# Performance work log

Measured on AMD Instinct MI355X. Metric: run time of the kernel, lower is better.

The kernel has to match this reference:

```python
import jax, jax.numpy as jnp
import numpy as np

IN_FEATURES = 4096
OUT_FEATURES = 11008
GROUP_SIZE = 128
NUM_GROUPS = IN_FEATURES // GROUP_SIZE


def setup_inputs() -> dict:
    key = jax.random.key(0)
    k1, k2, k3, k4 = jax.random.split(key, 4)
    x = jax.random.normal(k1, (4, 2048, IN_FEATURES), dtype=jnp.float32)
    qweight = jax.random.randint(k2, (OUT_FEATURES, NUM_GROUPS, GROUP_SIZE), 0, 16, dtype=jnp.int32).astype(jnp.int8)
    scales = jax.random.uniform(k3, (OUT_FEATURES, NUM_GROUPS), dtype=jnp.float32) * 0.02
    zeros = jax.random.uniform(k4, (OUT_FEATURES, NUM_GROUPS), dtype=jnp.float32) * 15.0
    return {"x": x, "qweight": qweight, "scales": scales, "zeros": zeros}


def reference(x, qweight, scales, zeros) -> jnp.ndarray:
    # Dequantize: (q - zero) * scale per (out_feature, group), then dense matmul.
    # qweight: [O, G, S], scales/zeros: [O, G] -> weight: [O, in]
    w = (qweight.astype(jnp.float32) - zeros[:, :, None]) * scales[:, :, None]
    w = w.reshape(OUT_FEATURES, IN_FEATURES)
    # x: [B, T, in] @ w.T -> [B, T, out]
    return jnp.einsum('bti,oi->bto', x, w)
```

## Files before the change

kernel.cpp:

```cpp
#include <hip/hip_runtime.h>
#include <hip/hip_bf16.h>
#include <stdint.h>


#define M_DIM 8192
#define K_DIM 4096
#define N_DIM 11008

typedef _Float16 f16x8 __attribute__((ext_vector_type(8)));
typedef float f32x4 __attribute__((ext_vector_type(4)));

__device__ __forceinline__ bool q_is_int8(const void* q) {
  const unsigned* w = (const unsigned*)q;
  unsigned m = 0;
#pragma unroll
  for (int i = 0; i < 16; ++i) m |= w[i] & 0xFFFFFF00u;
  return m != 0u;
}

__global__ void cvt_x_kernel(const float* __restrict__ X, _Float16* __restrict__ Xh, long total) {
  long e = ((long)blockIdx.x * blockDim.x + threadIdx.x) * 8;
  const long stride = (long)gridDim.x * blockDim.x * 8;
  for (; e < total; e += stride) {
    const float4 a = *(const float4*)(X + e);
    const float4 b = *(const float4*)(X + e + 4);
    f16x8 o;
    o[0] = (_Float16)a.x; o[1] = (_Float16)a.y; o[2] = (_Float16)a.z; o[3] = (_Float16)a.w;
    o[4] = (_Float16)b.x; o[5] = (_Float16)b.y; o[6] = (_Float16)b.z; o[7] = (_Float16)b.w;
    *(f16x8*)(Xh + e) = o;
  }
}

__global__ void dequant_w_kernel(const void* __restrict__ qraw,
                                 const float* __restrict__ scales,
                                 const float* __restrict__ zeros,
                                 _Float16* __restrict__ W) {
  const bool is8 = q_is_int8(qraw);
  const long total = (long)N_DIM * K_DIM;
  long e = ((long)blockIdx.x * blockDim.x + threadIdx.x) * 8;
  const long stride = (long)gridDim.x * blockDim.x * 8;
  for (; e < total; e += stride) {
    const long g = e >> 7;
    const float s = scales[g];
    const float z = zeros[g];
    float v[8];
    if (is8) {
      const uint2 p = *(const uint2*)((const uint8_t*)qraw + e);
      const unsigned a = p.x, b = p.y;
      v[0] = (float)(a & 0xFF);         v[1] = (float)((a >> 8) & 0xFF);
      v[2] = (float)((a >> 16) & 0xFF); v[3] = (float)(a >> 24);
      v[4] = (float)(b & 0xFF);         v[5] = (float)((b >> 8) & 0xFF);
      v[6] = (float)((b >> 16) & 0xFF); v[7] = (float)(b >> 24);
    } else {
      const int* qi = (const int*)qraw;
      const int4 p0 = *(const int4*)(qi + e);
      const int4 p1 = *(const int4*)(qi + e + 4);
      v[0] = (float)p0.x; v[1] = (float)p0.y; v[2] = (float)p0.z; v[3] = (float)p0.w;
      v[4] = (float)p1.x; v[5] = (float)p1.y; v[6] = (float)p1.z; v[7] = (float)p1.w;
    }
    f16x8 o;
#pragma unroll
    for (int k = 0; k < 8; ++k) o[k] = (_Float16)((v[k] - z) * s);
    *(f16x8*)(W + e) = o;
  }
}

__global__ __launch_bounds__(512, 2) void gemm_f16_pipe(
    const _Float16* __restrict__ A, const _Float16* __restrict__ B,
    float* __restrict__ C) {
  __shared__ __align__(16) _Float16 As[4][8192];
  __shared__ __align__(16) _Float16 Bs[4][8192];

  const int t = threadIdx.x;
  const int sw = ((blockIdx.x & 7) * 172) + (blockIdx.x >> 3);
  const int bm = sw & 31;
  const int bn = sw >> 5;

  const int w = t >> 6, l = t & 63;
  const int wm = w >> 2, wn = w & 3;
  const int fr = l & 15;
  const int cph = (l >> 4) << 3;

  const int sr = t >> 2;
  const int sc = (t & 3) << 3;
  const _Float16* Ag = A + (size_t)(bm * 256 + sr) * K_DIM + sc;
  const _Float16* Bg = B + (size_t)(bn * 256 + sr) * K_DIM + sc;

  f32x4 acc[8][4] = {};

#define AS1 const __attribute__((address_space(1))) void*
#define AS3 __attribute__((address_space(3))) void*
#define STAGE(kt, bf) do { \
    __builtin_amdgcn_global_load_lds((AS1)(Ag + (kt)), (AS3)(&As[bf][t * 8]), 16, 0, 0); \
    __builtin_amdgcn_global_load_lds((AS1)(Ag + 128 * K_DIM + (kt)), (AS3)(&As[bf][4096 + t * 8]), 16, 0, 0); \
    __builtin_amdgcn_global_load_lds((AS1)(Bg + (kt)), (AS3)(&Bs[bf][t * 8]), 16, 0, 0); \
    __builtin_amdgcn_global_load_lds((AS1)(Bg + 128 * K_DIM + (kt)), (AS3)(&Bs[bf][4096 + t * 8]), 16, 0, 0); \
  } while (0)

#define COMPUTE(bf) do { \
    const _Float16* Ap = &As[bf][(wm * 128 + fr) * 32 + cph]; \
    const _Float16* Bp = &Bs[bf][(wn * 64 + fr) * 32 + cph]; \
    f16x8 af[8]; f16x8 bg[4]; \
    _Pragma("unroll") for (int m = 0; m < 8; ++m) af[m] = *(const f16x8*)(Ap + m * 512); \
    _Pragma("unroll") for (int n = 0; n < 4; ++n) bg[n] = *(const f16x8*)(Bp + n * 512); \
    __builtin_amdgcn_s_setprio(1); \
    _Pragma("unroll") for (int m = 0; m < 8; ++m) \
      _Pragma("unroll") for (int n = 0; n < 4; ++n) \
        acc[m][n] = __builtin_amdgcn_mfma_f32_16x16x32_f16(af[m], bg[n], acc[m][n], 0, 0, 0); \
    __builtin_amdgcn_s_setprio(0); \
  } while (0)

#define WAITV(nimm) asm volatile("s_waitcnt vmcnt(" #nimm ")" ::: "memory")
#define BARRIER() do { __builtin_amdgcn_s_barrier(); asm volatile("" ::: "memory"); } while (0)

  STAGE(0, 0); STAGE(32, 1); STAGE(64, 2);
  WAITV(8);
  BARRIER();

  int kt = 96;
#pragma unroll 1
  for (int it = 0; it < 31; ++it) {
    STAGE(kt, 3);       COMPUTE(0); WAITV(8); BARRIER();
    STAGE(kt + 32, 0);  COMPUTE(1); WAITV(8); BARRIER();
    STAGE(kt + 64, 1);  COMPUTE(2); WAITV(8); BARRIER();
    STAGE(kt + 96, 2);  COMPUTE(3); WAITV(8); BARRIER();
    kt += 128;
  }
  STAGE(4064, 3); COMPUTE(0); WAITV(8); BARRIER();
  COMPUTE(1); WAITV(4); BARRIER();
  COMPUTE(2); WAITV(0); BARRIER();
  COMPUTE(3);

  const int qrow = (l >> 4) * 2;
  float* Cb = C + (size_t)(bm * 256 + wm * 128 + (l >> 4) * 4) * N_DIM + bn * 256 + wn * 64 + fr;
  (void)qrow;
#pragma unroll
  for (int m = 0; m < 8; ++m)
#pragma unroll
    for (int r = 0; r < 4; ++r) {
      float* Cr = Cb + (size_t)(m * 16 + r) * N_DIM;
#pragma unroll
      for (int n = 0; n < 4; ++n) Cr[n * 16] = acc[m][n][r];
    }
#undef STAGE
#undef COMPUTE
#undef WAITV
#undef BARRIER
#undef AS1
#undef AS3
}

extern "C" void kernel_launch(void* const* d_in, const int* in_sizes, int n_in,
                              void* d_out, int out_size, void* d_ws, size_t ws_size,
                              hipStream_t stream) {
  const float* x      = (const float*)d_in[0];
  const void*  qw     = d_in[1];
  const float* scales = (const float*)d_in[2];
  const float* zeros  = (const float*)d_in[3];
  float* out = (float*)d_out;

  const size_t xh_bytes = (size_t)M_DIM * K_DIM * sizeof(_Float16);
  const size_t wh_bytes = (size_t)N_DIM * K_DIM * sizeof(_Float16);
  if (ws_size < xh_bytes + wh_bytes) return;

  _Float16* Xh = (_Float16*)d_ws;
  _Float16* Wh = (_Float16*)((char*)d_ws + xh_bytes);

  cvt_x_kernel<<<2048, 256, 0, stream>>>(x, Xh, (long)M_DIM * K_DIM);
  dequant_w_kernel<<<2048, 256, 0, stream>>>(qw, scales, zeros, Wh);

  gemm_f16_pipe<<<dim3((M_DIM / 256) * (N_DIM / 256)), 512, 0, stream>>>(Xh, Wh, out);
}
```

Before: 1.386 ms.

## Restructure f16 GEMM into 8-phase double-buffered pipeline with swizzled LDS

Replaces the four-stage K=32 ring buffer with two K=64 buffers and an eight-phase schedule. Each phase interleaves partial LDS fragment reads, staggered global-to-LDS loads and a half-tile of MFMAs between barriers. An XOR swizzle on the LDS column chunks is meant to avoid bank conflicts on the wider 64-element rows. The added barriers and the tail-loop wraparound loads (masked kt) increase synchronization and issue a few redundant loads at the end in exchange for finer overlap.

Result: faster. 1.280 ms (-7.7%).

```diff
diff --git a/kernel.cpp b/kernel.cpp
--- a/kernel.cpp
+++ b/kernel.cpp
@@ -65,11 +65,11 @@
   }
 }
 
-__global__ __launch_bounds__(512, 2) void gemm_f16_pipe(
+__global__ __launch_bounds__(512, 2) void gemm_f16_8ph(
     const _Float16* __restrict__ A, const _Float16* __restrict__ B,
     float* __restrict__ C) {
-  __shared__ __align__(16) _Float16 As[4][8192];
-  __shared__ __align__(16) _Float16 Bs[4][8192];
+  __shared__ __align__(16) _Float16 As[2][16384];
+  __shared__ __align__(16) _Float16 Bs[2][16384];
 
   const int t = threadIdx.x;
   const int sw = ((blockIdx.x & 7) * 172) + (blockIdx.x >> 3);
@@ -79,61 +79,99 @@
   const int w = t >> 6, l = t & 63;
   const int wm = w >> 2, wn = w & 3;
   const int fr = l & 15;
-  const int cph = (l >> 4) << 3;
-
-  const int sr = t >> 2;
-  const int sc = (t & 3) << 3;
-  const _Float16* Ag = A + (size_t)(bm * 256 + sr) * K_DIM + sc;
-  const _Float16* Bg = B + (size_t)(bn * 256 + sr) * K_DIM + sc;
+  const int hi = l >> 4;
+  const int sx = fr & 7;
+
+  const int sl0 = ((hi) ^ sx) * 8;
+  const int sl1 = ((4 + hi) ^ sx) * 8;
+  const int arow = (wm * 128 + fr) * 64;
+  const int brow = (wn * 64 + fr) * 64;
+
+  const int tr = t >> 3;
+  const int ss = ((t & 7) ^ (tr & 7)) * 8;
+  const _Float16* Ag = A + (size_t)(bm * 256 + tr) * K_DIM + ss;
+  const _Float16* Bg = B + (size_t)(bn * 256 + tr) * K_DIM + ss;
 
   f32x4 acc[8][4] = {};
+  f16x8 af[4], bg0[4], bg1[4];
 
 #define AS1 const __attribute__((address_space(1))) void*
 #define AS3 __attribute__((address_space(3))) void*
-#define STAGE(kt, bf) do { \
-    __builtin_amdgcn_global_load_lds((AS1)(Ag + (kt)), (AS3)(&As[bf][t * 8]), 16, 0, 0); \
-    __builtin_amdgcn_global_load_lds((AS1)(Ag + 128 * K_DIM + (kt)), (AS3)(&As[bf][4096 + t * 8]), 16, 0, 0); \
-    __builtin_amdgcn_global_load_lds((AS1)(Bg + (kt)), (AS3)(&Bs[bf][t * 8]), 16, 0, 0); \
-    __builtin_amdgcn_global_load_lds((AS1)(Bg + 128 * K_DIM + (kt)), (AS3)(&Bs[bf][4096 + t * 8]), 16, 0, 0); \
-  } while (0)
-
-#define COMPUTE(bf) do { \
-    const _Float16* Ap = &As[bf][(wm * 128 + fr) * 32 + cph]; \
-    const _Float16* Bp = &Bs[bf][(wn * 64 + fr) * 32 + cph]; \
-    f16x8 af[8]; f16x8 bg[4]; \
-    _Pragma("unroll") for (int m = 0; m < 8; ++m) af[m] = *(const f16x8*)(Ap + m * 512); \
-    _Pragma("unroll") for (int n = 0; n < 4; ++n) bg[n] = *(const f16x8*)(Bp + n * 512); \
+#define STAGE_A(b, kt) do { \
+    __builtin_amdgcn_global_load_lds((AS1)(Ag + (kt)),                 (AS3)(&As[b][t * 8]), 16, 0, 0); \
+    __builtin_amdgcn_global_load_lds((AS1)(Ag +  64 * K_DIM + (kt)),   (AS3)(&As[b][4096 + t * 8]), 16, 0, 0); \
+    __builtin_amdgcn_global_load_lds((AS1)(Ag + 128 * K_DIM + (kt)),   (AS3)(&As[b][8192 + t * 8]), 16, 0, 0); \
+    __builtin_amdgcn_global_load_lds((AS1)(Ag + 192 * K_DIM + (kt)),   (AS3)(&As[b][12288 + t * 8]), 16, 0, 0); \
+  } while (0)
+#define STAGE_B_LO(b, kt) do { \
+    __builtin_amdgcn_global_load_lds((AS1)(Bg + (kt)),                 (AS3)(&Bs[b][t * 8]), 16, 0, 0); \
+    __builtin_amdgcn_global_load_lds((AS1)(Bg +  64 * K_DIM + (kt)),   (AS3)(&Bs[b][4096 + t * 8]), 16, 0, 0); \
+  } while (0)
+#define STAGE_B_HI(b, kt) do { \
+    __builtin_amdgcn_global_load_lds((AS1)(Bg + 128 * K_DIM + (kt)),   (AS3)(&Bs[b][8192 + t * 8]), 16, 0, 0); \
+    __builtin_amdgcn_global_load_lds((AS1)(Bg + 192 * K_DIM + (kt)),   (AS3)(&Bs[b][12288 + t * 8]), 16, 0, 0); \
+  } while (0)
+
+#define LDA(b, q, sl) do { \
+    af[0] = *(const f16x8*)(&As[b][arow + (q) * 4096 + (sl)]); \
+    af[1] = *(const f16x8*)(&As[b][arow + (q) * 4096 + 1024 + (sl)]); \
+    af[2] = *(const f16x8*)(&As[b][arow + (q) * 4096 + 2048 + (sl)]); \
+    af[3] = *(const f16x8*)(&As[b][arow + (q) * 4096 + 3072 + (sl)]); \
+  } while (0)
+#define LDB(b, dst, sl) do { \
+    dst[0] = *(const f16x8*)(&Bs[b][brow + (sl)]); \
+    dst[1] = *(const f16x8*)(&Bs[b][brow + 1024 + (sl)]); \
+    dst[2] = *(const f16x8*)(&Bs[b][brow + 2048 + (sl)]); \
+    dst[3] = *(const f16x8*)(&Bs[b][brow + 3072 + (sl)]); \
+  } while (0)
+
+#define MM(q, bgv) do { \
     __builtin_amdgcn_s_setprio(1); \
-    _Pragma("unroll") for (int m = 0; m < 8; ++m) \
+    _Pragma("unroll") for (int mi = 0; mi < 4; ++mi) \
       _Pragma("unroll") for (int n = 0; n < 4; ++n) \
-        acc[m][n] = __builtin_amdgcn_mfma_f32_16x16x32_f16(af[m], bg[n], acc[m][n], 0, 0, 0); \
+        acc[(q) * 4 + mi][n] = __builtin_amdgcn_mfma_f32_16x16x32_f16(af[mi], bgv[n], acc[(q) * 4 + mi][n], 0, 0, 0); \
     __builtin_amdgcn_s_setprio(0); \
   } while (0)
 
-#define WAITV(nimm) asm volatile("s_waitcnt vmcnt(" #nimm ")" ::: "memory")
-#define BARRIER() do { __builtin_amdgcn_s_barrier(); asm volatile("" ::: "memory"); } while (0)
-
-  STAGE(0, 0); STAGE(32, 1); STAGE(64, 2);
-  WAITV(8);
-  BARRIER();
-
-  int kt = 96;
+#define BAR() do { asm volatile("" ::: "memory"); __builtin_amdgcn_s_barrier(); asm volatile("" ::: "memory"); } while (0)
+#define WAITV(n) asm volatile("s_waitcnt vmcnt(" #n ")" ::: "memory")
+
+  STAGE_A(0, 0);
+  STAGE_B_LO(0, 0); STAGE_B_HI(0, 0);
+  STAGE_B_LO(1, 64); STAGE_B_HI(1, 64);
+  WAITV(4);
+  BAR();
+
 #pragma unroll 1
-  for (int it = 0; it < 31; ++it) {
-    STAGE(kt, 3);       COMPUTE(0); WAITV(8); BARRIER();
-    STAGE(kt + 32, 0);  COMPUTE(1); WAITV(8); BARRIER();
-    STAGE(kt + 64, 1);  COMPUTE(2); WAITV(8); BARRIER();
-    STAGE(kt + 96, 2);  COMPUTE(3); WAITV(8); BARRIER();
-    kt += 128;
+  for (int i = 0; i < 32; ++i) {
+    const int ktA1 = i * 128 + 64;
+    const int ktN2 = (i * 128 + 128) & 4095;
+    const int ktN3 = (i * 128 + 192) & 4095;
+    LDA(0, 0, sl0); LDB(0, bg0, sl0);
+    STAGE_A(1, ktA1);
+    BAR(); MM(0, bg0); BAR();
+    LDA(0, 0, sl1); LDB(0, bg1, sl1);
+    BAR(); MM(0, bg1); BAR();
+    LDA(0, 1, sl0);
+    STAGE_B_LO(0, ktN2);
+    BAR(); MM(1, bg0); BAR();
+    LDA(0, 1, sl1);
+    STAGE_B_HI(0, ktN2);
+    BAR(); MM(1, bg1); WAITV(4); BAR();
+    LDA(1, 0, sl0); LDB(1, bg0, sl0);
+    STAGE_A(0, ktN2);
+    BAR(); MM(0, bg0); BAR();
+    LDA(1, 0, sl1); LDB(1, bg1, sl1);
+    BAR(); MM(0, bg1); BAR();
+    LDA(1, 1, sl0);
+    STAGE_B_LO(1, ktN3);
+    BAR(); MM(1, bg0); BAR();
+    LDA(1, 1, sl1);
+    STAGE_B_HI(1, ktN3);
+    BAR(); MM(1, bg1); WAITV(4); BAR();
   }
-  STAGE(4064, 3); COMPUTE(0); WAITV(8); BARRIER();
-  COMPUTE(1); WAITV(4); BARRIER();
-  COMPUTE(2); WAITV(0); BARRIER();
-  COMPUTE(3);
-
-  const int qrow = (l >> 4) * 2;
-  float* Cb = C + (size_t)(bm * 256 + wm * 128 + (l >> 4) * 4) * N_DIM + bn * 256 + wn * 64 + fr;
-  (void)qrow;
+
+  float* Cb = C + (size_t)(bm * 256 + wm * 128 + hi * 4) * N_DIM + bn * 256 + wn * 64 + fr;
 #pragma unroll
   for (int m = 0; m < 8; ++m)
 #pragma unroll
@@ -142,10 +180,14 @@
 #pragma unroll
       for (int n = 0; n < 4; ++n) Cr[n * 16] = acc[m][n][r];
     }
-#undef STAGE
-#undef COMPUTE
+#undef STAGE_A
+#undef STAGE_B_LO
+#undef STAGE_B_HI
+#undef LDA
+#undef LDB
+#undef MM
+#undef BAR
 #undef WAITV
-#undef BARRIER
 #undef AS1
 #undef AS3
 }
@@ -169,5 +211,5 @@
   cvt_x_kernel<<<2048, 256, 0, stream>>>(x, Xh, (long)M_DIM * K_DIM);
   dequant_w_kernel<<<2048, 256, 0, stream>>>(qw, scales, zeros, Wh);
 
-  gemm_f16_pipe<<<dim3((M_DIM / 256) * (N_DIM / 256)), 512, 0, stream>>>(Xh, Wh, out);
-}
+  gemm_f16_8ph<<<dim3((M_DIM / 256) * (N_DIM / 256)), 512, 0, stream>>>(Xh, Wh, out);
+}
```

## Rewrite GEMM mainloop with 32x32x16 MFMA, XOR-swizzled LDS and split staging

Applied to the files above, without the earlier changes.

The f16 GEMM moves from 16x16x32 MFMAs with a 4-stage 32-wide K pipeline to 32x32x16 MFMAs over 64-wide K tiles with double buffering. LDS rows are XOR-swizzled to avoid bank conflicts, and A/B half-tile loads are interleaved between four MFMA phases, separated by barriers. The aim is higher MFMA efficiency and fewer LDS reads per flop. The cost is extra barriers per tile and shallower prefetch depth, which may expose memory latency.

New measurement: 1.400 ms. No clear change (+1.0%).

```diff
diff --git a/kernel.cpp b/kernel.cpp
--- a/kernel.cpp
+++ b/kernel.cpp
@@ -8,7 +8,7 @@
 #define N_DIM 11008
 
 typedef _Float16 f16x8 __attribute__((ext_vector_type(8)));
-typedef float f32x4 __attribute__((ext_vector_type(4)));
+typedef float f32x16 __attribute__((ext_vector_type(16)));
 
 __device__ __forceinline__ bool q_is_int8(const void* q) {
   const unsigned* w = (const unsigned*)q;
@@ -65,11 +65,11 @@
   }
 }
 
-__global__ __launch_bounds__(512, 2) void gemm_f16_pipe(
+__global__ __launch_bounds__(512, 2) void gemm_f16_3232(
     const _Float16* __restrict__ A, const _Float16* __restrict__ B,
     float* __restrict__ C) {
-  __shared__ __align__(16) _Float16 As[4][8192];
-  __shared__ __align__(16) _Float16 Bs[4][8192];
+  __shared__ __align__(16) _Float16 As[2][16384];
+  __shared__ __align__(16) _Float16 Bs[2][16384];
 
   const int t = threadIdx.x;
   const int sw = ((blockIdx.x & 7) * 172) + (blockIdx.x >> 3);
@@ -78,74 +78,121 @@
 
   const int w = t >> 6, l = t & 63;
   const int wm = w >> 2, wn = w & 3;
-  const int fr = l & 15;
-  const int cph = (l >> 4) << 3;
-
-  const int sr = t >> 2;
-  const int sc = (t & 3) << 3;
-  const _Float16* Ag = A + (size_t)(bm * 256 + sr) * K_DIM + sc;
-  const _Float16* Bg = B + (size_t)(bn * 256 + sr) * K_DIM + sc;
-
-  f32x4 acc[8][4] = {};
+  const int l31 = l & 31, hi2 = l >> 5;
+  const int s7 = l31 & 7;
+  const int sl0 = ((0 + hi2) ^ s7) * 8;
+  const int sl1 = ((2 + hi2) ^ s7) * 8;
+  const int sl2 = ((4 + hi2) ^ s7) * 8;
+  const int sl3 = ((6 + hi2) ^ s7) * 8;
+  const int Abase = (wm * 128 + l31) * 64;
+  const int Bbase = (wn * 64 + l31) * 64;
+
+  const int tr = t >> 3;
+  const int ss = ((t & 7) ^ (tr & 7)) * 8;
+  const _Float16* Ag = A + (size_t)(bm * 256 + tr) * K_DIM + ss;
+  const _Float16* Bg = B + (size_t)(bn * 256 + tr) * K_DIM + ss;
+
+  f32x16 acc[4][2] = {};
+  f16x8 af0, af1, af2, af3;
+  f16x8 bg00, bg10, bg01, bg11, bg02, bg12, bg03, bg13;
 
 #define AS1 const __attribute__((address_space(1))) void*
 #define AS3 __attribute__((address_space(3))) void*
-#define STAGE(kt, bf) do { \
-    __builtin_amdgcn_global_load_lds((AS1)(Ag + (kt)), (AS3)(&As[bf][t * 8]), 16, 0, 0); \
-    __builtin_amdgcn_global_load_lds((AS1)(Ag + 128 * K_DIM + (kt)), (AS3)(&As[bf][4096 + t * 8]), 16, 0, 0); \
-    __builtin_amdgcn_global_load_lds((AS1)(Bg + (kt)), (AS3)(&Bs[bf][t * 8]), 16, 0, 0); \
-    __builtin_amdgcn_global_load_lds((AS1)(Bg + 128 * K_DIM + (kt)), (AS3)(&Bs[bf][4096 + t * 8]), 16, 0, 0); \
+#define GLL(src, dst) __builtin_amdgcn_global_load_lds((AS1)(src), (AS3)(dst), 16, 0, 0)
+#define STAGE_A_LO(b, kt) do { GLL(Ag + (kt), &As[b][t * 8]); \
+                               GLL(Ag + 64 * K_DIM + (kt), &As[b][4096 + t * 8]); } while (0)
+#define STAGE_A_HI(b, kt) do { GLL(Ag + 128 * K_DIM + (kt), &As[b][8192 + t * 8]); \
+                               GLL(Ag + 192 * K_DIM + (kt), &As[b][12288 + t * 8]); } while (0)
+#define STAGE_B_LO(b, kt) do { GLL(Bg + (kt), &Bs[b][t * 8]); \
+                               GLL(Bg + 64 * K_DIM + (kt), &Bs[b][4096 + t * 8]); } while (0)
+#define STAGE_B_HI(b, kt) do { GLL(Bg + 128 * K_DIM + (kt), &Bs[b][8192 + t * 8]); \
+                               GLL(Bg + 192 * K_DIM + (kt), &Bs[b][12288 + t * 8]); } while (0)
+
+#define LDA(b, SL) do { \
+    af0 = *(const f16x8*)(&As[b][Abase + (SL)]); \
+    af1 = *(const f16x8*)(&As[b][Abase + 2048 + (SL)]); \
+    af2 = *(const f16x8*)(&As[b][Abase + 4096 + (SL)]); \
+    af3 = *(const f16x8*)(&As[b][Abase + 6144 + (SL)]); } while (0)
+#define LDB(b, ni, SL) (*(const f16x8*)(&Bs[b][Bbase + (ni) * 2048 + (SL)]))
+
+#define MM(b0, b1) do { \
+    __builtin_amdgcn_s_setprio(1); \
+    acc[0][0] = __builtin_amdgcn_mfma_f32_32x32x16_f16(af0, b0, acc[0][0], 0, 0, 0); \
+    acc[0][1] = __builtin_amdgcn_mfma_f32_32x32x16_f16(af0, b1, acc[0][1], 0, 0, 0); \
+    acc[1][0] = __builtin_amdgcn_mfma_f32_32x32x16_f16(af1, b0, acc[1][0], 0, 0, 0); \
+    acc[1][1] = __builtin_amdgcn_mfma_f32_32x32x16_f16(af1, b1, acc[1][1], 0, 0, 0); \
+    acc[2][0] = __builtin_amdgcn_mfma_f32_32x32x16_f16(af2, b0, acc[2][0], 0, 0, 0); \
+    acc[2][1] = __builtin_amdgcn_mfma_f32_32x32x16_f16(af2, b1, acc[2][1], 0, 0, 0); \
+    acc[3][0] = __builtin_amdgcn_mfma_f32_32x32x16_f16(af3, b0, acc[3][0], 0, 0, 0); \
+    acc[3][1] = __builtin_amdgcn_mfma_f32_32x32x16_f16(af3, b1, acc[3][1], 0, 0, 0); \
+    __builtin_amdgcn_s_setprio(0); } while (0)
+
+#define BAR() do { asm volatile("" ::: "memory"); __builtin_amdgcn_s_barrier(); asm volatile("" ::: "memory"); } while (0)
+#define WAITV(n) asm volatile("s_waitcnt vmcnt(" #n ")" ::: "memory")
+
+  STAGE_A_LO(0, 0); STAGE_A_HI(0, 0);
+  STAGE_B_LO(0, 0); STAGE_B_HI(0, 0);
+  STAGE_B_LO(1, 64); STAGE_B_HI(1, 64);
+  WAITV(4);
+  BAR();
+
+#define TILE(buf, nbuf, ktA, ktB) do { \
+     \
+    LDA(buf, sl0); \
+    bg00 = LDB(buf, 0, sl0); bg10 = LDB(buf, 1, sl0); \
+    bg01 = LDB(buf, 0, sl1); bg11 = LDB(buf, 1, sl1); \
+    STAGE_A_LO(nbuf, ktA); \
+    BAR(); MM(bg00, bg10); BAR(); \
+     \
+    LDA(buf, sl1); \
+    bg02 = LDB(buf, 0, sl2); bg12 = LDB(buf, 1, sl2); \
+    bg03 = LDB(buf, 0, sl3); bg13 = LDB(buf, 1, sl3); \
+    STAGE_A_HI(nbuf, ktA); \
+    BAR(); MM(bg01, bg11); BAR(); \
+     \
+    LDA(buf, sl2); \
+    STAGE_B_LO(buf, ktB); \
+    BAR(); MM(bg02, bg12); BAR(); \
+     \
+    LDA(buf, sl3); \
+    STAGE_B_HI(buf, ktB); \
+    BAR(); MM(bg03, bg13); WAITV(4); BAR(); \
   } while (0)
 
-#define COMPUTE(bf) do { \
-    const _Float16* Ap = &As[bf][(wm * 128 + fr) * 32 + cph]; \
-    const _Float16* Bp = &Bs[bf][(wn * 64 + fr) * 32 + cph]; \
-    f16x8 af[8]; f16x8 bg[4]; \
-    _Pragma("unroll") for (int m = 0; m < 8; ++m) af[m] = *(const f16x8*)(Ap + m * 512); \
-    _Pragma("unroll") for (int n = 0; n < 4; ++n) bg[n] = *(const f16x8*)(Bp + n * 512); \
-    __builtin_amdgcn_s_setprio(1); \
-    _Pragma("unroll") for (int m = 0; m < 8; ++m) \
-      _Pragma("unroll") for (int n = 0; n < 4; ++n) \
-        acc[m][n] = __builtin_amdgcn_mfma_f32_16x16x32_f16(af[m], bg[n], acc[m][n], 0, 0, 0); \
-    __builtin_amdgcn_s_setprio(0); \
-  } while (0)
-
-#define WAITV(nimm) asm volatile("s_waitcnt vmcnt(" #nimm ")" ::: "memory")
-#define BARRIER() do { __builtin_amdgcn_s_barrier(); asm volatile("" ::: "memory"); } while (0)
-
-  STAGE(0, 0); STAGE(32, 1); STAGE(64, 2);
-  WAITV(8);
-  BARRIER();
-
-  int kt = 96;
 #pragma unroll 1
-  for (int it = 0; it < 31; ++it) {
-    STAGE(kt, 3);       COMPUTE(0); WAITV(8); BARRIER();
-    STAGE(kt + 32, 0);  COMPUTE(1); WAITV(8); BARRIER();
-    STAGE(kt + 64, 1);  COMPUTE(2); WAITV(8); BARRIER();
-    STAGE(kt + 96, 2);  COMPUTE(3); WAITV(8); BARRIER();
-    kt += 128;
+  for (int T = 0; T < 64; T += 2) {
+    const int ktA0 = ((T + 1) & 63) * 64;
+    const int ktB0 = ((T + 2) & 63) * 64;
+    TILE(0, 1, ktA0, ktB0);
+    const int ktA1 = ((T + 2) & 63) * 64;
+    const int ktB1 = ((T + 3) & 63) * 64;
+    TILE(1, 0, ktA1, ktB1);
   }
-  STAGE(4064, 3); COMPUTE(0); WAITV(8); BARRIER();
-  COMPUTE(1); WAITV(4); BARRIER();
-  COMPUTE(2); WAITV(0); BARRIER();
-  COMPUTE(3);
-
-  const int qrow = (l >> 4) * 2;
-  float* Cb = C + (size_t)(bm * 256 + wm * 128 + (l >> 4) * 4) * N_DIM + bn * 256 + wn * 64 + fr;
-  (void)qrow;
-#pragma unroll
-  for (int m = 0; m < 8; ++m)
-#pragma unroll
-    for (int r = 0; r < 4; ++r) {
-      float* Cr = Cb + (size_t)(m * 16 + r) * N_DIM;
-#pragma unroll
-      for (int n = 0; n < 4; ++n) Cr[n * 16] = acc[m][n][r];
+
+  const int r0 = bm * 256 + wm * 128 + 4 * hi2;
+  const int c0 = bn * 256 + wn * 64 + l31;
+#pragma unroll
+  for (int mi = 0; mi < 4; ++mi)
+#pragma unroll
+    for (int ni = 0; ni < 2; ++ni) {
+      float* Cf = C + (size_t)(r0 + mi * 32) * N_DIM + c0 + ni * 32;
+#pragma unroll
+      for (int reg = 0; reg < 16; ++reg) {
+        const int rr = (reg & 3) + 8 * (reg >> 2);
+        Cf[(size_t)rr * N_DIM] = acc[mi][ni][reg];
+      }
     }
-#undef STAGE
-#undef COMPUTE
+#undef TILE
+#undef STAGE_A_LO
+#undef STAGE_A_HI
+#undef STAGE_B_LO
+#undef STAGE_B_HI
+#undef LDA
+#undef LDB
+#undef MM
+#undef BAR
 #undef WAITV
-#undef BARRIER
+#undef GLL
 #undef AS1
 #undef AS3
 }
@@ -169,5 +216,5 @@
   cvt_x_kernel<<<2048, 256, 0, stream>>>(x, Xh, (long)M_DIM * K_DIM);
   dequant_w_kernel<<<2048, 256, 0, stream>>>(qw, scales, zeros, Wh);
 
-  gemm_f16_pipe<<<dim3((M_DIM / 256) * (N_DIM / 256)), 512, 0, stream>>>(Xh, Wh, out);
-}
+  gemm_f16_3232<<<dim3((M_DIM / 256) * (N_DIM / 256)), 512, 0, stream>>>(Xh, Wh, out);
+}
```
